# Optimization experiments

Measured on AMD Instinct MI355X. Metric: run time of the kernel, lower is better.

Reference implementation:

```python
import jax, jax.numpy as jnp
import numpy as np

HIDDEN = 4096
INTER = 11008
GROUP = 128  # group_size (group_size_shift = 7)
EPS = 1e-6


def _group_dequant(q, sm):
    # q: [out, in] int; sm: [out, G, 2] with sm[...,0]=scale, sm[...,1]=min_val
    out_dim, in_dim = q.shape
    G = in_dim // GROUP
    qf = q.astype(jnp.float32).reshape(out_dim, G, GROUP)
    w = qf * sm[:, :, 0:1] + sm[:, :, 1:2]
    return w.reshape(out_dim, in_dim)


def _rmsnorm(x, w, eps):
    var = jnp.mean(x * x, axis=-1, keepdims=True)
    return x * jax.lax.rsqrt(var + eps) * w


def setup_inputs() -> dict:
    key = jax.random.key(0)
    ks = jax.random.split(key, 8)
    inp = jax.random.normal(ks[0], (4, 32, HIDDEN), dtype=jnp.float32)
    residual = jax.random.normal(ks[1], (4, 32, HIDDEN), dtype=jnp.float32)
    norm_weights = jax.random.uniform(ks[2], (HIDDEN,), dtype=jnp.float32, minval=0.5, maxval=1.5)
    gate_up_q = jax.random.randint(ks[3], (INTER, HIDDEN, 2), 0, 256, dtype=jnp.int32)
    g_gu = HIDDEN // GROUP  # 32
    gu_scale = jax.random.uniform(ks[4], (INTER, 2, g_gu, 1), dtype=jnp.float32, minval=1e-4, maxval=2e-3)
    gu_min = -127.5 * gu_scale + 1e-3 * jax.random.normal(ks[5], (INTER, 2, g_gu, 1), dtype=jnp.float32)
    gate_up_sm = jnp.concatenate([gu_scale, gu_min], axis=-1)
    down_q = jax.random.randint(ks[6], (HIDDEN, INTER), 0, 256, dtype=jnp.int32)
    g_d = INTER // GROUP  # 86
    kd = jax.random.split(ks[7], 2)
    d_scale = jax.random.uniform(kd[0], (HIDDEN, g_d, 1), dtype=jnp.float32, minval=1e-4, maxval=2e-3)
    d_min = -127.5 * d_scale + 1e-3 * jax.random.normal(kd[1], (HIDDEN, g_d, 1), dtype=jnp.float32)
    down_sm = jnp.concatenate([d_scale, d_min], axis=-1)
    return {"input": inp, "residual": residual, "norm_weights": norm_weights,
            "gate_up_q": gate_up_q, "gate_up_sm": gate_up_sm,
            "down_q": down_q, "down_sm": down_sm}


def reference(input, residual, norm_weights, gate_up_q, gate_up_sm, down_q, down_sm):
    x = _rmsnorm(input, norm_weights, EPS)
    # dequantize packed gate/up weights: [INTER, HIDDEN] each
    gate_w = _group_dequant(gate_up_q[:, :, 0], gate_up_sm[:, 0])
    up_w = _group_dequant(gate_up_q[:, :, 1], gate_up_sm[:, 1])
    down_w = _group_dequant(down_q, down_sm)  # [HIDDEN, INTER]
    g = jnp.einsum('bsh,ih->bsi', x, gate_w)
    u = jnp.einsum('bsh,ih->bsi', x, up_w)
    h = jax.nn.silu(g) * u
    out = jnp.einsum('bsi,hi->bsh', h, down_w)
    return out + residual
```

## Files before the change

### kernel.cpp

```cpp
#include <hip/hip_runtime.h>
#include <math.h>

#define HIDDEN 4096
#define INTER  11008
#define NTOK   128

typedef _Float16 half8 __attribute__((ext_vector_type(8)));
typedef float    f32x4 __attribute__((ext_vector_type(4)));

__device__ __forceinline__ f32x4 mfma16(half8 a, half8 b, f32x4 c) {
  return __builtin_amdgcn_mfma_f32_16x16x32_f16(a, b, c, 0, 0, 0);
}

__device__ __forceinline__ _Float16 dq1(int v, float s, float m) {
  return (_Float16)((float)v * s + m);
}

__global__ __launch_bounds__(256) void k_rmsnorm(const float* __restrict__ in,
                                                 const float* __restrict__ nw,
                                                 _Float16* __restrict__ xo) {
  const int tok = blockIdx.x;
  const int tid = threadIdx.x;
  const float* row = in + (size_t)tok * HIDDEN;
  float4 v[4];
  float ss = 0.f;
#pragma unroll
  for (int j = 0; j < 4; ++j) {
    v[j] = *(const float4*)&row[tid * 4 + j * 1024];
    ss += v[j].x * v[j].x + v[j].y * v[j].y + v[j].z * v[j].z + v[j].w * v[j].w;
  }
#pragma unroll
  for (int o = 32; o; o >>= 1) ss += __shfl_xor(ss, o);
  __shared__ float wsum[4];
  if ((tid & 63) == 0) wsum[tid >> 6] = ss;
  __syncthreads();
  ss = wsum[0] + wsum[1] + wsum[2] + wsum[3];
  const float rs = rsqrtf(ss * (1.f / HIDDEN) + 1e-6f);
#pragma unroll
  for (int j = 0; j < 4; ++j) {
    const int k = tid * 4 + j * 1024;
    const float4 w = *(const float4*)&nw[k];
    union { _Float16 h[4]; uint2 u; } p;
    p.h[0] = (_Float16)(v[j].x * rs * w.x);
    p.h[1] = (_Float16)(v[j].y * rs * w.y);
    p.h[2] = (_Float16)(v[j].z * rs * w.z);
    p.h[3] = (_Float16)(v[j].w * rs * w.w);
    *(uint2*)&xo[(size_t)tok * HIDDEN + k] = p.u;
  }
}

__global__ __launch_bounds__(256) void k_gateup(const _Float16* __restrict__ x,
                                                const int* __restrict__ q,
                                                const float* __restrict__ sm,
                                                _Float16* __restrict__ h) {
  const int tid   = threadIdx.x;
  const int lane  = tid & 63;
  const int wave  = tid >> 6;
  const int colt  = wave & 1;
  const int khalf = wave >> 1;
  const int colbase = blockIdx.x * 32 + colt * 16;
  const int l15  = lane & 15;
  const int bcol = colbase + l15;
  const int koff = (lane >> 4) * 8;

  f32x4 aG[8], aU[8];
  const f32x4 zz = {0.f, 0.f, 0.f, 0.f};
#pragma unroll
  for (int m = 0; m < 8; ++m) { aG[m] = zz; aU[m] = zz; }

  const int*   qrow  = q  + (size_t)bcol * (HIDDEN * 2);
  const float* smrow = sm + (size_t)bcol * 128;

  for (int grp = khalf * 16; grp < khalf * 16 + 16; ++grp) {
    const float2 sg = *(const float2*)&smrow[grp * 2];
    const float2 su = *(const float2*)&smrow[64 + grp * 2];
#pragma unroll 2
    for (int t = 0; t < 4; ++t) {
      const int kb = grp * 128 + t * 32 + koff;
      const int4 b0 = *(const int4*)&qrow[(size_t)kb * 2 + 0];
      const int4 b1 = *(const int4*)&qrow[(size_t)kb * 2 + 4];
      const int4 b2 = *(const int4*)&qrow[(size_t)kb * 2 + 8];
      const int4 b3 = *(const int4*)&qrow[(size_t)kb * 2 + 12];
      half8 bg, bu;
      bg[0] = dq1(b0.x, sg.x, sg.y); bu[0] = dq1(b0.y, su.x, su.y);
      bg[1] = dq1(b0.z, sg.x, sg.y); bu[1] = dq1(b0.w, su.x, su.y);
      bg[2] = dq1(b1.x, sg.x, sg.y); bu[2] = dq1(b1.y, su.x, su.y);
      bg[3] = dq1(b1.z, sg.x, sg.y); bu[3] = dq1(b1.w, su.x, su.y);
      bg[4] = dq1(b2.x, sg.x, sg.y); bu[4] = dq1(b2.y, su.x, su.y);
      bg[5] = dq1(b2.z, sg.x, sg.y); bu[5] = dq1(b2.w, su.x, su.y);
      bg[6] = dq1(b3.x, sg.x, sg.y); bu[6] = dq1(b3.y, su.x, su.y);
      bg[7] = dq1(b3.z, sg.x, sg.y); bu[7] = dq1(b3.w, su.x, su.y);
      const _Float16* xp = x + kb;
#pragma unroll
      for (int m = 0; m < 8; ++m) {
        const half8 a = *(const half8*)&xp[(size_t)(m * 16 + l15) * HIDDEN];
        aG[m] = mfma16(a, bg, aG[m]);
        aU[m] = mfma16(a, bu, aU[m]);
      }
    }
  }

  __shared__ float red[2][8][2][64][4];
  if (khalf == 1) {
#pragma unroll
    for (int m = 0; m < 8; ++m) {
      *(f32x4*)&red[colt][m][0][lane][0] = aG[m];
      *(f32x4*)&red[colt][m][1][lane][0] = aU[m];
    }
  }
  __syncthreads();
  if (khalf == 0) {
    const int trow = (lane >> 4) * 4;
#pragma unroll
    for (int m = 0; m < 8; ++m) {
      const f32x4 g2 = *(const f32x4*)&red[colt][m][0][lane][0];
      const f32x4 u2 = *(const f32x4*)&red[colt][m][1][lane][0];
#pragma unroll
      for (int r = 0; r < 4; ++r) {
        const float g = aG[m][r] + g2[r];
        const float u = aU[m][r] + u2[r];
        const float hv = g / (1.f + __expf(-g)) * u;
        const int token = m * 16 + trow + r;
        h[(size_t)token * INTER + colbase + l15] = (_Float16)hv;
      }
    }
  }
}

__global__ __launch_bounds__(256) void k_down(const _Float16* __restrict__ h,
                                              const int* __restrict__ q,
                                              const float* __restrict__ sm,
                                              float* __restrict__ part) {
  const int tid   = threadIdx.x;
  const int lane  = tid & 63;
  const int wave  = tid >> 6;
  const int colt  = wave & 1;
  const int khalf = wave >> 1;
  const int ntile = blockIdx.x >> 2;
  const int kblk  = blockIdx.x & 3;
  const int colbase = ntile * 32 + colt * 16;
  const int l15  = lane & 15;
  const int bcol = colbase + l15;
  const int koff = (lane >> 4) * 8;
  const int KW   = INTER / 8;
  const int kstart = (kblk * 2 + khalf) * KW;

  f32x4 acc[8];
  const f32x4 zz = {0.f, 0.f, 0.f, 0.f};
#pragma unroll
  for (int m = 0; m < 8; ++m) acc[m] = zz;

  const int*   qrow  = q  + (size_t)bcol * INTER;
  const float* smrow = sm + (size_t)bcol * (86 * 2);

#pragma unroll 2
  for (int kk = 0; kk < KW / 32; ++kk) {
    const int k0 = kstart + kk * 32;
    const int kb = k0 + koff;
    const int grp = k0 >> 7;
    const float2 s = *(const float2*)&smrow[grp * 2];
    const int4 b0 = *(const int4*)&qrow[kb];
    const int4 b1 = *(const int4*)&qrow[kb + 4];
    half8 bw;
    bw[0] = dq1(b0.x, s.x, s.y);
    bw[1] = dq1(b0.y, s.x, s.y);
    bw[2] = dq1(b0.z, s.x, s.y);
    bw[3] = dq1(b0.w, s.x, s.y);
    bw[4] = dq1(b1.x, s.x, s.y);
    bw[5] = dq1(b1.y, s.x, s.y);
    bw[6] = dq1(b1.z, s.x, s.y);
    bw[7] = dq1(b1.w, s.x, s.y);
    const _Float16* hp = h + kb;
#pragma unroll
    for (int m = 0; m < 8; ++m) {
      const half8 a = *(const half8*)&hp[(size_t)(m * 16 + l15) * INTER];
      acc[m] = mfma16(a, bw, acc[m]);
    }
  }

  __shared__ float red[2][8][64][4];
  if (khalf == 1) {
#pragma unroll
    for (int m = 0; m < 8; ++m) *(f32x4*)&red[colt][m][lane][0] = acc[m];
  }
  __syncthreads();
  if (khalf == 0) {
    float* pb = part + (size_t)kblk * ((size_t)NTOK * HIDDEN);
    const int trow = (lane >> 4) * 4;
#pragma unroll
    for (int m = 0; m < 8; ++m) {
      const f32x4 o = *(const f32x4*)&red[colt][m][lane][0];
#pragma unroll
      for (int r = 0; r < 4; ++r) {
        const int token = m * 16 + trow + r;
        pb[(size_t)token * HIDDEN + colbase + l15] = acc[m][r] + o[r];
      }
    }
  }
}

__global__ __launch_bounds__(256) void k_final(const float* __restrict__ res,
                                               const float* __restrict__ part,
                                               float* __restrict__ out) {
  const int i = blockIdx.x * 256 + threadIdx.x;
#pragma unroll
  for (int j = 0; j < 2; ++j) {
    const size_t idx = ((size_t)j * 65536 + i) * 4;
    float4 a        = *(const float4*)&res[idx];
    const float4 p0 = *(const float4*)&part[idx];
    const float4 p1 = *(const float4*)&part[(size_t)1 * NTOK * HIDDEN + idx];
    const float4 p2 = *(const float4*)&part[(size_t)2 * NTOK * HIDDEN + idx];
    const float4 p3 = *(const float4*)&part[(size_t)3 * NTOK * HIDDEN + idx];
    a.x += p0.x + p1.x + p2.x + p3.x;
    a.y += p0.y + p1.y + p2.y + p3.y;
    a.z += p0.z + p1.z + p2.z + p3.z;
    a.w += p0.w + p1.w + p2.w + p3.w;
    *(float4*)&out[idx] = a;
  }
}

extern "C" void kernel_launch(void* const* d_in, const int* in_sizes, int n_in,
                              void* d_out, int out_size, void* d_ws, size_t ws_size,
                              hipStream_t stream) {
  const float* inp  = (const float*)d_in[0];
  const float* res  = (const float*)d_in[1];
  const float* nw   = (const float*)d_in[2];
  const int*   guq  = (const int*)d_in[3];
  const float* gusm = (const float*)d_in[4];
  const int*   dq   = (const int*)d_in[5];
  const float* dsm  = (const float*)d_in[6];
  float* out = (float*)d_out;

  char* ws = (char*)d_ws;
  _Float16* x    = (_Float16*)ws;
  _Float16* hbuf = (_Float16*)(ws + (1u << 20));
  float*    part = (float*)(ws + (4u << 20));

  k_rmsnorm<<<NTOK, 256, 0, stream>>>(inp, nw, x);
  k_gateup<<<INTER / 32, 256, 0, stream>>>(x, guq, gusm, hbuf);
  k_down<<<(HIDDEN / 32) * 4, 256, 0, stream>>>(hbuf, dq, dsm, part);
  k_final<<<256, 256, 0, stream>>>(res, part, out);
}
```

Measured before the change: 777.8 us.

## Split-K gate/up and down GEMMs across more blocks with separate reduction kernels

```diff
diff --git a/kernel.cpp b/kernel.cpp
--- a/kernel.cpp
+++ b/kernel.cpp
@@ -52,12 +52,14 @@
 __global__ __launch_bounds__(256) void k_gateup(const _Float16* __restrict__ x,
                                                 const int* __restrict__ q,
                                                 const float* __restrict__ sm,
-                                                _Float16* __restrict__ h) {
+                                                float* __restrict__ pg,
+                                                float* __restrict__ pu) {
   const int tid   = threadIdx.x;
   const int lane  = tid & 63;
   const int wave  = tid >> 6;
   const int colt  = wave & 1;
   const int khalf = wave >> 1;
+  const int ks    = blockIdx.y;
   const int colbase = blockIdx.x * 32 + colt * 16;
   const int l15  = lane & 15;
   const int bcol = colbase + l15;
@@ -71,7 +73,8 @@
   const int*   qrow  = q  + (size_t)bcol * (HIDDEN * 2);
   const float* smrow = sm + (size_t)bcol * 128;
 
-  for (int grp = khalf * 16; grp < khalf * 16 + 16; ++grp) {
+  const int grp0 = ks * 8 + khalf * 4;
+  for (int grp = grp0; grp < grp0 + 4; ++grp) {
     const float2 sg = *(const float2*)&smrow[grp * 2];
     const float2 su = *(const float2*)&smrow[64 + grp * 2];
 #pragma unroll 2
@@ -111,39 +114,59 @@
   __syncthreads();
   if (khalf == 0) {
     const int trow = (lane >> 4) * 4;
+    float* pgb = pg + (size_t)ks * NTOK * INTER;
+    float* pub = pu + (size_t)ks * NTOK * INTER;
 #pragma unroll
     for (int m = 0; m < 8; ++m) {
       const f32x4 g2 = *(const f32x4*)&red[colt][m][0][lane][0];
       const f32x4 u2 = *(const f32x4*)&red[colt][m][1][lane][0];
 #pragma unroll
       for (int r = 0; r < 4; ++r) {
-        const float g = aG[m][r] + g2[r];
-        const float u = aU[m][r] + u2[r];
-        const float hv = g / (1.f + __expf(-g)) * u;
         const int token = m * 16 + trow + r;
-        h[(size_t)token * INTER + colbase + l15] = (_Float16)hv;
+        pgb[(size_t)token * INTER + colbase + l15] = aG[m][r] + g2[r];
+        pub[(size_t)token * INTER + colbase + l15] = aU[m][r] + u2[r];
       }
     }
   }
+}
+
+__global__ __launch_bounds__(256) void k_silu(const float* __restrict__ pg,
+                                              const float* __restrict__ pu,
+                                              _Float16* __restrict__ h) {
+  const size_t base = ((size_t)blockIdx.x * 256 + threadIdx.x) * 8;
+  f32x4 g0 = {0,0,0,0}, g1 = {0,0,0,0}, u0 = {0,0,0,0}, u1 = {0,0,0,0};
+#pragma unroll
+  for (int ks = 0; ks < 4; ++ks) {
+    const float* pgb = pg + (size_t)ks * NTOK * INTER + base;
+    const float* pub = pu + (size_t)ks * NTOK * INTER + base;
+    g0 += *(const f32x4*)pgb; g1 += *(const f32x4*)(pgb + 4);
+    u0 += *(const f32x4*)pub; u1 += *(const f32x4*)(pub + 4);
+  }
+  union { _Float16 h[8]; uint4 u; } p;
+#pragma unroll
+  for (int j = 0; j < 4; ++j) {
+    p.h[j]     = (_Float16)(g0[j] / (1.f + __expf(-g0[j])) * u0[j]);
+    p.h[j + 4] = (_Float16)(g1[j] / (1.f + __expf(-g1[j])) * u1[j]);
+  }
+  *(uint4*)&h[base] = p.u;
 }
 
 __global__ __launch_bounds__(256) void k_down(const _Float16* __restrict__ h,
                                               const int* __restrict__ q,
                                               const float* __restrict__ sm,
-                                              float* __restrict__ part) {
+                                              float* __restrict__ pd) {
   const int tid   = threadIdx.x;
   const int lane  = tid & 63;
   const int wave  = tid >> 6;
   const int colt  = wave & 1;
   const int khalf = wave >> 1;
-  const int ntile = blockIdx.x >> 2;
-  const int kblk  = blockIdx.x & 3;
+  const int ntile = blockIdx.x;
+  const int ks    = blockIdx.y;
   const int colbase = ntile * 32 + colt * 16;
   const int l15  = lane & 15;
   const int bcol = colbase + l15;
   const int koff = (lane >> 4) * 8;
-  const int KW   = INTER / 8;
-  const int kstart = (kblk * 2 + khalf) * KW;
+  const int slot = ks * 2 + khalf;
 
   f32x4 acc[8];
   const f32x4 zz = {0.f, 0.f, 0.f, 0.f};
@@ -154,10 +177,9 @@
   const float* smrow = sm + (size_t)bcol * (86 * 2);
 
 #pragma unroll 2
-  for (int kk = 0; kk < KW / 32; ++kk) {
-    const int k0 = kstart + kk * 32;
-    const int kb = k0 + koff;
-    const int grp = k0 >> 7;
+  for (int c = slot; c < 344; c += 16) {
+    const int kb = c * 32 + koff;
+    const int grp = c >> 2;
     const float2 s = *(const float2*)&smrow[grp * 2];
     const int4 b0 = *(const int4*)&qrow[kb];
     const int4 b1 = *(const int4*)&qrow[kb + 4];
@@ -185,7 +207,7 @@
   }
   __syncthreads();
   if (khalf == 0) {
-    float* pb = part + (size_t)kblk * ((size_t)NTOK * HIDDEN);
+    float* pb = pd + (size_t)ks * NTOK * HIDDEN;
     const int trow = (lane >> 4) * 4;
 #pragma unroll
     for (int m = 0; m < 8; ++m) {
@@ -200,23 +222,19 @@
 }
 
 __global__ __launch_bounds__(256) void k_final(const float* __restrict__ res,
-                                               const float* __restrict__ part,
+                                               const float* __restrict__ pd,
                                                float* __restrict__ out) {
-  const int i = blockIdx.x * 256 + threadIdx.x;
-#pragma unroll
-  for (int j = 0; j < 2; ++j) {
-    const size_t idx = ((size_t)j * 65536 + i) * 4;
-    float4 a        = *(const float4*)&res[idx];
-    const float4 p0 = *(const float4*)&part[idx];
-    const float4 p1 = *(const float4*)&part[(size_t)1 * NTOK * HIDDEN + idx];
-    const float4 p2 = *(const float4*)&part[(size_t)2 * NTOK * HIDDEN + idx];
-    const float4 p3 = *(const float4*)&part[(size_t)3 * NTOK * HIDDEN + idx];
-    a.x += p0.x + p1.x + p2.x + p3.x;
-    a.y += p0.y + p1.y + p2.y + p3.y;
-    a.z += p0.z + p1.z + p2.z + p3.z;
-    a.w += p0.w + p1.w + p2.w + p3.w;
-    *(float4*)&out[idx] = a;
-  }
+  const size_t base = ((size_t)blockIdx.x * 256 + threadIdx.x) * 8;
+  f32x4 a0 = *(const f32x4*)&res[base];
+  f32x4 a1 = *(const f32x4*)&res[base + 4];
+#pragma unroll
+  for (int ks = 0; ks < 8; ++ks) {
+    const float* p = pd + (size_t)ks * NTOK * HIDDEN + base;
+    a0 += *(const f32x4*)p;
+    a1 += *(const f32x4*)(p + 4);
+  }
+  *(f32x4*)&out[base] = a0;
+  *(f32x4*)&out[base + 4] = a1;
 }
 
 extern "C" void kernel_launch(void* const* d_in, const int* in_sizes, int n_in,
@@ -234,10 +252,13 @@
   char* ws = (char*)d_ws;
   _Float16* x    = (_Float16*)ws;
   _Float16* hbuf = (_Float16*)(ws + (1u << 20));
-  float*    part = (float*)(ws + (4u << 20));
+  float*    pg   = (float*)(ws + (4u << 20));
+  float*    pu   = (float*)(ws + (28u << 20));
+  float*    pd   = (float*)(ws + (52u << 20));
 
   k_rmsnorm<<<NTOK, 256, 0, stream>>>(inp, nw, x);
-  k_gateup<<<INTER / 32, 256, 0, stream>>>(x, guq, gusm, hbuf);
-  k_down<<<(HIDDEN / 32) * 4, 256, 0, stream>>>(hbuf, dq, dsm, part);
-  k_final<<<256, 256, 0, stream>>>(res, part, out);
-}
+  k_gateup<<<dim3(INTER / 32, 4), 256, 0, stream>>>(x, guq, gusm, pg, pu);
+  k_silu<<<(NTOK * INTER) / (256 * 8), 256, 0, stream>>>(pg, pu, hbuf);
+  k_down<<<dim3(HIDDEN / 32, 8), 256, 0, stream>>>(hbuf, dq, dsm, pd);
+  k_final<<<(NTOK * HIDDEN) / (256 * 8), 256, 0, stream>>>(res, pd, out);
+}
```

Result: slower. 794.2 us (+2.1%).
